# Performance work log

Hardware: AMD Instinct MI355X
Metric: run time of the kernel (lower is better)

Reference implementation:

```python
import jax, jax.numpy as jnp
import numpy as np

H, LQ, LK, DK, DV = 16, 2048, 2048, 64, 64


def setup_inputs() -> dict:
    key = jax.random.key(0)
    k1, k2, k3, k4 = jax.random.split(key, 4)
    q = jax.random.normal(k1, (H, LQ, DK), dtype=jnp.float32)
    k = jax.random.normal(k2, (H, LK, DK), dtype=jnp.float32)
    v = jax.random.normal(k3, (1, LK, DV), dtype=jnp.float32)
    attn_mask = jax.random.randint(k4, (H, LQ, LK), 0, 2) == 1
    return {"q": q, "k": k, "v": v, "attn_mask": attn_mask, "train_attn": 1}


def reference(q, k, v, attn_mask, train_attn):
    scale = jnp.asarray(np.sqrt(q.shape[-1]), q.dtype)  # sqrt(d_k)
    # [H, Lq, Lk] scores
    attn = jnp.einsum('hqd,hkd->hqk', q, k) / scale
    attn = jnp.where(attn_mask, -jnp.inf, attn)
    attn = jax.nn.softmax(attn, axis=-1)
    # torch: v.repeat(n_heads,1,1) then bmm -> v[0] broadcast over heads
    attn_used = attn if train_attn else jax.lax.stop_gradient(attn)
    v_used = jax.lax.stop_gradient(v) if train_attn else v
    outputs = jnp.einsum('hqk,kd->hqd', attn_used, v_used[0])
    return outputs, attn
```

## Files before the change

kernel.cpp:

```cpp
#include <hip/hip_runtime.h>
#include <hip/hip_bf16.h>
#include <math.h>

#define H_ 16
#define LQ_ 2048
#define LK_ 2048
#define D_ 64
#define MBLK_ 32
#define NWAVE_ 4
#define STRIP_ (LK_ / NWAVE_)
#define NCH_ (STRIP_ / 32)

using bf16x8  = __attribute__((ext_vector_type(8))) short;
using floatx4 = __attribute__((ext_vector_type(4))) float;

__device__ __forceinline__ unsigned short f2bf(float x) {
  unsigned u = __builtin_bit_cast(unsigned, x);
  return (unsigned short)((u + 0x7fffu + ((u >> 16) & 1u)) >> 16);
}
__device__ __forceinline__ float bf2f(unsigned short b) {
  return __builtin_bit_cast(float, ((unsigned)b) << 16);
}
__device__ __forceinline__ void hilo8(const float* __restrict__ x, bf16x8& hv, bf16x8& lv) {
#pragma unroll
  for (int j = 0; j < 8; ++j) {
    unsigned short hb = f2bf(x[j]);
    float d = x[j] - bf2f(hb);
    hv[j] = (short)hb;
    lv[j] = (short)(unsigned short)(__builtin_bit_cast(unsigned, d) >> 16);
  }
}

__global__ void detect_mask_kernel(const unsigned int* __restrict__ m,
                                   int* __restrict__ flag) {
  if (threadIdx.x == 0) {
    unsigned int acc = 0u;
#pragma unroll 8
    for (int i = 0; i < 256; ++i) acc |= m[i];
    *flag = (acc & 0xFFFFFF00u) ? 1 : 0;
  }
}

__global__ __launch_bounds__(256, 2)
void attn_mfma_kernel(const float* __restrict__ Qg, const float* __restrict__ Kg,
                      const float* __restrict__ Vg, const void* __restrict__ Mg,
                      const int* __restrict__ flagp,
                      float* __restrict__ Og, float* __restrict__ Ag) {
  const int tid = (int)threadIdx.x;
  const int l   = tid & 63;
  const int w   = tid >> 6;
  const int lm  = l & 15;
  const int lg  = l >> 4;
  const int hd  = (int)blockIdx.y;
  const int q0  = (int)blockIdx.x * MBLK_;
  const int k0w = w * STRIP_;

  __shared__ __align__(16) float OM[NWAVE_][MBLK_ * D_];
  __shared__ float Stats[NWAVE_][MBLK_][2];

  short* Pw = reinterpret_cast<short*>(&OM[0][0]) + w * 2048;
  short* Ph = Pw;
  short* Pl = Pw + 1024;

  const int maskByte = *flagp;
  const unsigned char* Mb = (const unsigned char*)Mg;
  const int* Mi = (const int*)Mg;

  const float* Qh_ = Qg + (size_t)hd * LQ_ * D_;
  const float* Kh_ = Kg + (size_t)hd * LK_ * D_;

  bf16x8 qh[2][2], ql[2][2];
#pragma unroll
  for (int Mt = 0; Mt < 2; ++Mt) {
    const float* qp = Qh_ + (size_t)(q0 + Mt * 16 + lm) * D_;
#pragma unroll
    for (int s = 0; s < 2; ++s) {
      float x[8];
      *(floatx4*)(x)     = *(const floatx4*)(qp + s * 32 + lg * 8);
      *(floatx4*)(x + 4) = *(const floatx4*)(qp + s * 32 + lg * 8 + 4);
      hilo8(x, qh[Mt][s], ql[Mt][s]);
    }
  }

  float mreg[8], sreg[8];
#pragma unroll
  for (int i = 0; i < 8; ++i) { mreg[i] = -1e30f; sreg[i] = 0.0f; }

#pragma unroll 1
  for (int c = 0; c < NCH_; ++c) {
#pragma unroll
    for (int kt = 0; kt < 2; ++kt) {
      const int kcol = k0w + c * 32 + kt * 16 + lm;
      const float* kp = Kh_ + (size_t)kcol * D_;
      bf16x8 kh[2], kl[2];
#pragma unroll
      for (int s = 0; s < 2; ++s) {
        float x[8];
        *(floatx4*)(x)     = *(const floatx4*)(kp + s * 32 + lg * 8);
        *(floatx4*)(x + 4) = *(const floatx4*)(kp + s * 32 + lg * 8 + 4);
        hilo8(x, kh[s], kl[s]);
      }
#pragma unroll
      for (int Mt = 0; Mt < 2; ++Mt) {
        floatx4 acc = {0.f, 0.f, 0.f, 0.f};
#pragma unroll
        for (int s = 0; s < 2; ++s) {
          acc = __builtin_amdgcn_mfma_f32_16x16x32_bf16(qh[Mt][s], kh[s], acc, 0, 0, 0);
          acc = __builtin_amdgcn_mfma_f32_16x16x32_bf16(ql[Mt][s], kh[s], acc, 0, 0, 0);
          acc = __builtin_amdgcn_mfma_f32_16x16x32_bf16(qh[Mt][s], kl[s], acc, 0, 0, 0);
        }
#pragma unroll
        for (int j = 0; j < 4; ++j) {
          const int row = Mt * 16 + lg * 4 + j;
          const size_t mi = ((size_t)hd * LQ_ + q0 + row) * (size_t)LK_ + kcol;
          const int msk = maskByte ? (int)Mb[mi] : Mi[mi];
          const float sv = msk ? -1e30f : acc[j] * 0.125f;
          const int rs = Mt * 4 + j;
          const float mo = mreg[rs];
          const float mn = fmaxf(mo, sv);
          sreg[rs] = sreg[rs] * __expf(mo - mn) + (msk ? 0.0f : __expf(sv - mn));
          mreg[rs] = mn;
        }
      }
    }
  }

#pragma unroll
  for (int rs = 0; rs < 8; ++rs) {
    float m = mreg[rs], S = sreg[rs];
#pragma unroll
    for (int off = 1; off <= 8; off <<= 1) {
      float mo = __shfl_xor(m, off, 64);
      float So = __shfl_xor(S, off, 64);
      float mn = fmaxf(m, mo);
      S = S * __expf(m - mn) + So * __expf(mo - mn);
      m = mn;
    }
    mreg[rs] = m; sreg[rs] = S;
  }
  if (lm == 0) {
#pragma unroll
    for (int rs = 0; rs < 8; ++rs) {
      const int row = (rs >> 2) * 16 + lg * 4 + (rs & 3);
      Stats[w][row][0] = mreg[rs];
      Stats[w][row][1] = sreg[rs];
    }
  }
  __syncthreads();
  float mfin[8], isum[8];
#pragma unroll
  for (int rs = 0; rs < 8; ++rs) {
    const int row = (rs >> 2) * 16 + lg * 4 + (rs & 3);
    float m = Stats[0][row][0], S = Stats[0][row][1];
#pragma unroll
    for (int ww = 1; ww < NWAVE_; ++ww) {
      float mo = Stats[ww][row][0], So = Stats[ww][row][1];
      float mn = fmaxf(m, mo);
      S = S * __expf(m - mn) + So * __expf(mo - mn);
      m = mn;
    }
    mfin[rs] = m; isum[rs] = 1.0f / S;
  }

  floatx4 oacc[2][4];
#pragma unroll
  for (int Mt = 0; Mt < 2; ++Mt)
#pragma unroll
    for (int Nt = 0; Nt < 4; ++Nt) oacc[Mt][Nt] = {0.f, 0.f, 0.f, 0.f};

#pragma unroll 1
  for (int c = 0; c < NCH_; ++c) {
    const int kc0 = k0w + c * 32;
#pragma unroll
    for (int kt = 0; kt < 2; ++kt) {
      const int kcol = kc0 + kt * 16 + lm;
      const float* kp = Kh_ + (size_t)kcol * D_;
      bf16x8 kh[2], kl[2];
#pragma unroll
      for (int s = 0; s < 2; ++s) {
        float x[8];
        *(floatx4*)(x)     = *(const floatx4*)(kp + s * 32 + lg * 8);
        *(floatx4*)(x + 4) = *(const floatx4*)(kp + s * 32 + lg * 8 + 4);
        hilo8(x, kh[s], kl[s]);
      }
#pragma unroll
      for (int Mt = 0; Mt < 2; ++Mt) {
        floatx4 acc = {0.f, 0.f, 0.f, 0.f};
#pragma unroll
        for (int s = 0; s < 2; ++s) {
          acc = __builtin_amdgcn_mfma_f32_16x16x32_bf16(qh[Mt][s], kh[s], acc, 0, 0, 0);
          acc = __builtin_amdgcn_mfma_f32_16x16x32_bf16(ql[Mt][s], kh[s], acc, 0, 0, 0);
          acc = __builtin_amdgcn_mfma_f32_16x16x32_bf16(qh[Mt][s], kl[s], acc, 0, 0, 0);
        }
#pragma unroll
        for (int j = 0; j < 4; ++j) {
          const int row = Mt * 16 + lg * 4 + j;
          const size_t mi = ((size_t)hd * LQ_ + q0 + row) * (size_t)LK_ + kcol;
          const int msk = maskByte ? (int)Mb[mi] : Mi[mi];
          const int rs = Mt * 4 + j;
          const float p = msk ? 0.0f : __expf(acc[j] * 0.125f - mfin[rs]) * isum[rs];
          Ag[mi] = p;
          const unsigned short phb = f2bf(p);
          Ph[row * 32 + kt * 16 + lm] = (short)phb;
          Pl[row * 32 + kt * 16 + lm] =
              (short)(unsigned short)(__builtin_bit_cast(unsigned, p - bf2f(phb)) >> 16);
        }
      }
    }
    bf16x8 pa[2], plo[2];
#pragma unroll
    for (int Mt = 0; Mt < 2; ++Mt) {
      pa[Mt]  = *(const bf16x8*)(Ph + (Mt * 16 + lm) * 32 + lg * 8);
      plo[Mt] = *(const bf16x8*)(Pl + (Mt * 16 + lm) * 32 + lg * 8);
    }
#pragma unroll
    for (int Nt = 0; Nt < 4; ++Nt) {
      float vx[8];
#pragma unroll
      for (int jj = 0; jj < 8; ++jj)
        vx[jj] = Vg[(size_t)(kc0 + lg * 8 + jj) * D_ + Nt * 16 + lm];
      bf16x8 vh, vl;
      hilo8(vx, vh, vl);
#pragma unroll
      for (int Mt = 0; Mt < 2; ++Mt) {
        floatx4 o = oacc[Mt][Nt];
        o = __builtin_amdgcn_mfma_f32_16x16x32_bf16(pa[Mt],  vh, o, 0, 0, 0);
        o = __builtin_amdgcn_mfma_f32_16x16x32_bf16(plo[Mt], vh, o, 0, 0, 0);
        o = __builtin_amdgcn_mfma_f32_16x16x32_bf16(pa[Mt],  vl, o, 0, 0, 0);
        oacc[Mt][Nt] = o;
      }
    }
  }

  __syncthreads();
#pragma unroll
  for (int Mt = 0; Mt < 2; ++Mt)
#pragma unroll
    for (int Nt = 0; Nt < 4; ++Nt)
#pragma unroll
      for (int j = 0; j < 4; ++j)
        OM[w][(Mt * 16 + lg * 4 + j) * D_ + Nt * 16 + lm] = oacc[Mt][Nt][j];
  __syncthreads();
  for (int i = tid; i < MBLK_ * D_; i += 256) {
    const float s0 = OM[0][i] + OM[1][i] + OM[2][i] + OM[3][i];
    Og[((size_t)hd * LQ_ + q0 + (i >> 6)) * D_ + (i & 63)] = s0;
  }
}

extern "C" void kernel_launch(void* const* d_in, const int* in_sizes, int n_in,
                              void* d_out, int out_size, void* d_ws, size_t ws_size,
                              hipStream_t stream) {
  const float* Qg = (const float*)d_in[0];
  const float* Kg = (const float*)d_in[1];
  const float* Vg = (const float*)d_in[2];
  const void*  Mg = d_in[3];
  int* flag = (int*)d_ws;

  hipLaunchKernelGGL(detect_mask_kernel, dim3(1), dim3(64), 0, stream,
                     (const unsigned int*)Mg, flag);

  float* Og = (float*)d_out;
  float* Ag = (float*)d_out + (size_t)H_ * LQ_ * D_;

  dim3 grid(LQ_ / MBLK_, H_);
  hipLaunchKernelGGL(attn_mfma_kernel, grid, dim3(256), 0, stream,
                     Qg, Kg, Vg, Mg, flag, Og, Ag);
}
```

Baseline: 799.7 us.

## Precompute bf16 hi/lo operands and packed bitmask, single-pass score kernel

Adds pre-kernels that pack the mask into bits, split Q and K into bf16 hi/lo arrays, and transpose V into hi/lo bf16. The attention kernel now uses 16-row query blocks, keeps all scores in registers so QK^T is computed once instead of twice, uses an exact max/sum softmax, and writes the attention matrix with vectorized stores. This removes the recomputed QK^T, the repeated per-use conversions, and the byte-wide mask reads, at the cost of extra launches, workspace traffic and higher register use. Attention values are now stored as hi+lo bf16 sums, which may differ slightly from fp32.

```diff
diff --git a/kernel.cpp b/kernel.cpp
--- a/kernel.cpp
+++ b/kernel.cpp
@@ -6,10 +6,12 @@
 #define LQ_ 2048
 #define LK_ 2048
 #define D_ 64
-#define MBLK_ 32
-#define NWAVE_ 4
-#define STRIP_ (LK_ / NWAVE_)
+#define QB_ 16
+#define NW_ 4
+#define STRIP_ (LK_ / NW_)
+#define NTL_ (STRIP_ / 16)
 #define NCH_ (STRIP_ / 32)
+#define PP_ 40
 
 using bf16x8  = __attribute__((ext_vector_type(8))) short;
 using floatx4 = __attribute__((ext_vector_type(4))) float;
@@ -31,219 +33,256 @@
   }
 }
 
-__global__ void detect_mask_kernel(const unsigned int* __restrict__ m,
-                                   int* __restrict__ flag) {
-  if (threadIdx.x == 0) {
-    unsigned int acc = 0u;
-#pragma unroll 8
-    for (int i = 0; i < 256; ++i) acc |= m[i];
-    *flag = (acc & 0xFFFFFF00u) ? 1 : 0;
-  }
-}
-
+__global__ void detect_mask_kernel(const unsigned* __restrict__ m, int* __restrict__ flag) {
+  const int l = (int)threadIdx.x;
+  unsigned acc = 0;
+#pragma unroll
+  for (int i = 0; i < 4; ++i) acc |= m[l * 4 + i];
+  unsigned long long any = __ballot(acc & 0xFFFFFF00u);
+  if (l == 0) *flag = any ? 1 : 0;
+}
+
+__global__ void pack_mask_kernel(const void* __restrict__ Mg, const int* __restrict__ flagp,
+                                 unsigned* __restrict__ Wp) {
+  const size_t i = (size_t)blockIdx.x * 256 + threadIdx.x;
+  unsigned wbits = 0;
+  if (*flagp) {
+    const uint4* p = (const uint4*)((const unsigned char*)Mg + i * 32);
+    uint4 a = p[0], b = p[1];
+    unsigned v[8] = {a.x, a.y, a.z, a.w, b.x, b.y, b.z, b.w};
+#pragma unroll
+    for (int k = 0; k < 8; ++k)
+#pragma unroll
+      for (int bb = 0; bb < 4; ++bb)
+        wbits |= (((v[k] >> (8 * bb)) & 0xFFu) ? 1u : 0u) << (4 * k + bb);
+  } else {
+    const uint4* p = (const uint4*)((const int*)Mg + i * 32);
+#pragma unroll
+    for (int k = 0; k < 8; ++k) {
+      uint4 a = p[k];
+      wbits |= (a.x ? 1u : 0u) << (4 * k)     | (a.y ? 1u : 0u) << (4 * k + 1) |
+               (a.z ? 1u : 0u) << (4 * k + 2) | (a.w ? 1u : 0u) << (4 * k + 3);
+    }
+  }
+  Wp[i] = wbits;
+}
+
+__global__ void conv_hilo_kernel(const float* __restrict__ X,
+                                 unsigned short* __restrict__ Hh,
+                                 unsigned short* __restrict__ Hl) {
+  const size_t i = (size_t)blockIdx.x * 256 + threadIdx.x;
+  float x[8];
+  *(floatx4*)x       = *(const floatx4*)(X + i * 8);
+  *(floatx4*)(x + 4) = *(const floatx4*)(X + i * 8 + 4);
+  bf16x8 hv, lv;
+  hilo8(x, hv, lv);
+  *(bf16x8*)(Hh + i * 8) = hv;
+  *(bf16x8*)(Hl + i * 8) = lv;
+}
+
+__global__ void conv_vt_kernel(const float* __restrict__ V,
+                               unsigned short* __restrict__ Th,
+                               unsigned short* __restrict__ Tl) {
+  const int i = (int)(blockIdx.x * 256 + threadIdx.x);
+  const int d = i >> 11, k = i & 2047;
+  float x = V[(size_t)k * D_ + d];
+  unsigned short hb = f2bf(x);
+  float rem = x - bf2f(hb);
+  Th[(size_t)d * LK_ + k] = hb;
+  Tl[(size_t)d * LK_ + k] = (unsigned short)(__builtin_bit_cast(unsigned, rem) >> 16);
+}
+
+template <bool PRE>
 __global__ __launch_bounds__(256, 2)
-void attn_mfma_kernel(const float* __restrict__ Qg, const float* __restrict__ Kg,
-                      const float* __restrict__ Vg, const void* __restrict__ Mg,
-                      const int* __restrict__ flagp,
-                      float* __restrict__ Og, float* __restrict__ Ag) {
+void attn_sp_kernel(const float* __restrict__ Qg, const float* __restrict__ Kg,
+                    const float* __restrict__ Vg, const void* __restrict__ Mg,
+                    const int* __restrict__ flagp,
+                    const unsigned* __restrict__ Wp,
+                    const unsigned short* __restrict__ Qhp, const unsigned short* __restrict__ Qlp,
+                    const unsigned short* __restrict__ Khp, const unsigned short* __restrict__ Klp,
+                    const unsigned short* __restrict__ Vthp, const unsigned short* __restrict__ Vtlp,
+                    float* __restrict__ Og, float* __restrict__ Ag) {
   const int tid = (int)threadIdx.x;
-  const int l   = tid & 63;
-  const int w   = tid >> 6;
-  const int lm  = l & 15;
-  const int lg  = l >> 4;
-  const int hd  = (int)blockIdx.y;
-  const int q0  = (int)blockIdx.x * MBLK_;
-  const int k0w = w * STRIP_;
-
-  __shared__ __align__(16) float OM[NWAVE_][MBLK_ * D_];
-  __shared__ float Stats[NWAVE_][MBLK_][2];
-
-  short* Pw = reinterpret_cast<short*>(&OM[0][0]) + w * 2048;
-  short* Ph = Pw;
-  short* Pl = Pw + 1024;
-
-  const int maskByte = *flagp;
+  const int l = tid & 63, w = tid >> 6, lm = l & 15, lg = l >> 4;
+  const int hd = (int)blockIdx.y;
+  const int q0 = (int)blockIdx.x * QB_;
+  const int k0 = w * STRIP_;
+
+  __shared__ float SM_[NW_][QB_];
+  __shared__ float SS_[NW_][QB_];
+  __shared__ __align__(16) float OM[NW_][QB_ * D_];
+  __shared__ __align__(16) unsigned short Pb[NW_][2][QB_ * PP_];
+
+  const int maskByte = PRE ? 0 : *flagp;
   const unsigned char* Mb = (const unsigned char*)Mg;
   const int* Mi = (const int*)Mg;
 
-  const float* Qh_ = Qg + (size_t)hd * LQ_ * D_;
-  const float* Kh_ = Kg + (size_t)hd * LK_ * D_;
-
-  bf16x8 qh[2][2], ql[2][2];
-#pragma unroll
-  for (int Mt = 0; Mt < 2; ++Mt) {
-    const float* qp = Qh_ + (size_t)(q0 + Mt * 16 + lm) * D_;
+  bf16x8 qh[2], ql[2];
+  if constexpr (PRE) {
+    const unsigned short* qp  = Qhp + ((size_t)hd * LQ_ + q0 + lm) * D_;
+    const unsigned short* qp2 = Qlp + ((size_t)hd * LQ_ + q0 + lm) * D_;
+    qh[0] = *(const bf16x8*)(qp + lg * 8);       qh[1] = *(const bf16x8*)(qp + 32 + lg * 8);
+    ql[0] = *(const bf16x8*)(qp2 + lg * 8);      ql[1] = *(const bf16x8*)(qp2 + 32 + lg * 8);
+  } else {
+    const float* qp = Qg + ((size_t)hd * LQ_ + q0 + lm) * D_;
 #pragma unroll
     for (int s = 0; s < 2; ++s) {
       float x[8];
-      *(floatx4*)(x)     = *(const floatx4*)(qp + s * 32 + lg * 8);
+      *(floatx4*)x       = *(const floatx4*)(qp + s * 32 + lg * 8);
       *(floatx4*)(x + 4) = *(const floatx4*)(qp + s * 32 + lg * 8 + 4);
-      hilo8(x, qh[Mt][s], ql[Mt][s]);
-    }
-  }
-
-  float mreg[8], sreg[8];
-#pragma unroll
-  for (int i = 0; i < 8; ++i) { mreg[i] = -1e30f; sreg[i] = 0.0f; }
-
-#pragma unroll 1
+      hilo8(x, qh[s], ql[s]);
+    }
+  }
+
+  float s[NTL_][4];
+  unsigned wm[4];
+  const size_t mwrow = ((size_t)hd * LQ_ + q0 + lg * 4);
+#pragma unroll
+  for (int t = 0; t < NTL_; ++t) {
+    if constexpr (PRE) {
+      if ((t & 1) == 0) {
+#pragma unroll
+        for (int j = 0; j < 4; ++j)
+          wm[j] = Wp[((mwrow + j) << 6) + (size_t)(w * 16) + (t >> 1)];
+      }
+    }
+    bf16x8 kh[2], kl[2];
+    if constexpr (PRE) {
+      const unsigned short* kp  = Khp + ((size_t)hd * LK_ + k0 + t * 16 + lm) * D_;
+      const unsigned short* kp2 = Klp + ((size_t)hd * LK_ + k0 + t * 16 + lm) * D_;
+      kh[0] = *(const bf16x8*)(kp + lg * 8);       kh[1] = *(const bf16x8*)(kp + 32 + lg * 8);
+      kl[0] = *(const bf16x8*)(kp2 + lg * 8);      kl[1] = *(const bf16x8*)(kp2 + 32 + lg * 8);
+    } else {
+      const float* kp = Kg + ((size_t)hd * LK_ + k0 + t * 16 + lm) * D_;
+#pragma unroll
+      for (int ss = 0; ss < 2; ++ss) {
+        float x[8];
+        *(floatx4*)x       = *(const floatx4*)(kp + ss * 32 + lg * 8);
+        *(floatx4*)(x + 4) = *(const floatx4*)(kp + ss * 32 + lg * 8 + 4);
+        hilo8(x, kh[ss], kl[ss]);
+      }
+    }
+    floatx4 acc = {0.f, 0.f, 0.f, 0.f};
+#pragma unroll
+    for (int ss = 0; ss < 2; ++ss) {
+      acc = __builtin_amdgcn_mfma_f32_16x16x32_bf16(qh[ss], kh[ss], acc, 0, 0, 0);
+      acc = __builtin_amdgcn_mfma_f32_16x16x32_bf16(ql[ss], kh[ss], acc, 0, 0, 0);
+      acc = __builtin_amdgcn_mfma_f32_16x16x32_bf16(qh[ss], kl[ss], acc, 0, 0, 0);
+    }
+#pragma unroll
+    for (int j = 0; j < 4; ++j) {
+      int mk;
+      if constexpr (PRE) {
+        mk = (int)((wm[j] >> ((t & 1) * 16 + lm)) & 1u);
+      } else {
+        const size_t mi = ((size_t)hd * LQ_ + q0 + lg * 4 + j) * (size_t)LK_ + k0 + t * 16 + lm;
+        mk = maskByte ? (int)Mb[mi] : Mi[mi];
+      }
+      s[t][j] = mk ? -1e30f : acc[j] * 0.125f;
+    }
+  }
+
+  float mf[4];
+#pragma unroll
+  for (int j = 0; j < 4; ++j) {
+    float m = s[0][j];
+#pragma unroll
+    for (int t = 1; t < NTL_; ++t) m = fmaxf(m, s[t][j]);
+#pragma unroll
+    for (int off = 1; off <= 8; off <<= 1) m = fmaxf(m, __shfl_xor(m, off, 64));
+    if (lm == 0) SM_[w][lg * 4 + j] = m;
+  }
+  __syncthreads();
+#pragma unroll
+  for (int j = 0; j < 4; ++j)
+    mf[j] = fmaxf(fmaxf(SM_[0][lg * 4 + j], SM_[1][lg * 4 + j]),
+                  fmaxf(SM_[2][lg * 4 + j], SM_[3][lg * 4 + j]));
+#pragma unroll
+  for (int j = 0; j < 4; ++j) {
+    float sum = 0.f;
+#pragma unroll
+    for (int t = 0; t < NTL_; ++t) {
+      float p = __expf(s[t][j] - mf[j]);
+      s[t][j] = p;
+      sum += p;
+    }
+#pragma unroll
+    for (int off = 1; off <= 8; off <<= 1) sum += __shfl_xor(sum, off, 64);
+    if (lm == 0) SS_[w][lg * 4 + j] = sum;
+  }
+  __syncthreads();
+  float inv[4];
+#pragma unroll
+  for (int j = 0; j < 4; ++j)
+    inv[j] = 1.0f / (SS_[0][lg * 4 + j] + SS_[1][lg * 4 + j] +
+                     SS_[2][lg * 4 + j] + SS_[3][lg * 4 + j]);
+
+  floatx4 oacc[4];
+#pragma unroll
+  for (int n = 0; n < 4; ++n) oacc[n] = {0.f, 0.f, 0.f, 0.f};
+  unsigned short* PhL = &Pb[w][0][0];
+  unsigned short* PlL = &Pb[w][1][0];
+
+#pragma unroll
   for (int c = 0; c < NCH_; ++c) {
 #pragma unroll
-    for (int kt = 0; kt < 2; ++kt) {
-      const int kcol = k0w + c * 32 + kt * 16 + lm;
-      const float* kp = Kh_ + (size_t)kcol * D_;
-      bf16x8 kh[2], kl[2];
-#pragma unroll
-      for (int s = 0; s < 2; ++s) {
-        float x[8];
-        *(floatx4*)(x)     = *(const floatx4*)(kp + s * 32 + lg * 8);
-        *(floatx4*)(x + 4) = *(const floatx4*)(kp + s * 32 + lg * 8 + 4);
-        hilo8(x, kh[s], kl[s]);
-      }
-#pragma unroll
-      for (int Mt = 0; Mt < 2; ++Mt) {
-        floatx4 acc = {0.f, 0.f, 0.f, 0.f};
-#pragma unroll
-        for (int s = 0; s < 2; ++s) {
-          acc = __builtin_amdgcn_mfma_f32_16x16x32_bf16(qh[Mt][s], kh[s], acc, 0, 0, 0);
-          acc = __builtin_amdgcn_mfma_f32_16x16x32_bf16(ql[Mt][s], kh[s], acc, 0, 0, 0);
-          acc = __builtin_amdgcn_mfma_f32_16x16x32_bf16(qh[Mt][s], kl[s], acc, 0, 0, 0);
-        }
-#pragma unroll
-        for (int j = 0; j < 4; ++j) {
-          const int row = Mt * 16 + lg * 4 + j;
-          const size_t mi = ((size_t)hd * LQ_ + q0 + row) * (size_t)LK_ + kcol;
-          const int msk = maskByte ? (int)Mb[mi] : Mi[mi];
-          const float sv = msk ? -1e30f : acc[j] * 0.125f;
-          const int rs = Mt * 4 + j;
-          const float mo = mreg[rs];
-          const float mn = fmaxf(mo, sv);
-          sreg[rs] = sreg[rs] * __expf(mo - mn) + (msk ? 0.0f : __expf(sv - mn));
-          mreg[rs] = mn;
-        }
-      }
-    }
-  }
-
-#pragma unroll
-  for (int rs = 0; rs < 8; ++rs) {
-    float m = mreg[rs], S = sreg[rs];
-#pragma unroll
-    for (int off = 1; off <= 8; off <<= 1) {
-      float mo = __shfl_xor(m, off, 64);
-      float So = __shfl_xor(S, off, 64);
-      float mn = fmaxf(m, mo);
-      S = S * __expf(m - mn) + So * __expf(mo - mn);
-      m = mn;
-    }
-    mreg[rs] = m; sreg[rs] = S;
-  }
-  if (lm == 0) {
-#pragma unroll
-    for (int rs = 0; rs < 8; ++rs) {
-      const int row = (rs >> 2) * 16 + lg * 4 + (rs & 3);
-      Stats[w][row][0] = mreg[rs];
-      Stats[w][row][1] = sreg[rs];
-    }
-  }
+    for (int u = 0; u < 2; ++u) {
+#pragma unroll
+      for (int j = 0; j < 4; ++j) {
+        const float p = s[2 * c + u][j] * inv[j];
+        const unsigned short hb = f2bf(p);
+        const float rem = p - bf2f(hb);
+        PhL[(lg * 4 + j) * PP_ + u * 16 + lm] = hb;
+        PlL[(lg * 4 + j) * PP_ + u * 16 + lm] =
+            (unsigned short)(__builtin_bit_cast(unsigned, rem) >> 16);
+      }
+    }
+    const bf16x8 pa  = *(const bf16x8*)(PhL + lm * PP_ + lg * 8);
+    const bf16x8 plo = *(const bf16x8*)(PlL + lm * PP_ + lg * 8);
+
+    {
+      float pr[8];
+#pragma unroll
+      for (int jj = 0; jj < 8; ++jj)
+        pr[jj] = bf2f((unsigned short)pa[jj]) + bf2f((unsigned short)plo[jj]);
+      float* arow = Ag + ((size_t)hd * LQ_ + q0 + lm) * (size_t)LK_ + k0 + c * 32 + lg * 8;
+      floatx4 v0 = {pr[0], pr[1], pr[2], pr[3]};
+      floatx4 v1 = {pr[4], pr[5], pr[6], pr[7]};
+      *(floatx4*)arow       = v0;
+      *(floatx4*)(arow + 4) = v1;
+    }
+
+#pragma unroll
+    for (int n = 0; n < 4; ++n) {
+      bf16x8 vh, vl;
+      if constexpr (PRE) {
+        const size_t vo = (size_t)(n * 16 + lm) * LK_ + k0 + c * 32 + lg * 8;
+        vh = *(const bf16x8*)(Vthp + vo);
+        vl = *(const bf16x8*)(Vtlp + vo);
+      } else {
+        float vx[8];
+#pragma unroll
+        for (int jj = 0; jj < 8; ++jj)
+          vx[jj] = Vg[(size_t)(k0 + c * 32 + lg * 8 + jj) * D_ + n * 16 + lm];
+        hilo8(vx, vh, vl);
+      }
+      floatx4 o = oacc[n];
+      o = __builtin_amdgcn_mfma_f32_16x16x32_bf16(pa,  vh, o, 0, 0, 0);
+      o = __builtin_amdgcn_mfma_f32_16x16x32_bf16(plo, vh, o, 0, 0, 0);
+      o = __builtin_amdgcn_mfma_f32_16x16x32_bf16(pa,  vl, o, 0, 0, 0);
+      oacc[n] = o;
+    }
+  }
+
+#pragma unroll
+  for (int n = 0; n < 4; ++n)
+#pragma unroll
+    for (int j = 0; j < 4; ++j)
+      OM[w][(lg * 4 + j) * D_ + n * 16 + lm] = oacc[n][j];
   __syncthreads();
-  float mfin[8], isum[8];
-#pragma unroll
-  for (int rs = 0; rs < 8; ++rs) {
-    const int row = (rs >> 2) * 16 + lg * 4 + (rs & 3);
-    float m = Stats[0][row][0], S = Stats[0][row][1];
-#pragma unroll
-    for (int ww = 1; ww < NWAVE_; ++ww) {
-      float mo = Stats[ww][row][0], So = Stats[ww][row][1];
-      float mn = fmaxf(m, mo);
-      S = S * __expf(m - mn) + So * __expf(mo - mn);
-      m = mn;
-    }
-    mfin[rs] = m; isum[rs] = 1.0f / S;
-  }
-
-  floatx4 oacc[2][4];
-#pragma unroll
-  for (int Mt = 0; Mt < 2; ++Mt)
-#pragma unroll
-    for (int Nt = 0; Nt < 4; ++Nt) oacc[Mt][Nt] = {0.f, 0.f, 0.f, 0.f};
-
-#pragma unroll 1
-  for (int c = 0; c < NCH_; ++c) {
-    const int kc0 = k0w + c * 32;
-#pragma unroll
-    for (int kt = 0; kt < 2; ++kt) {
-      const int kcol = kc0 + kt * 16 + lm;
-      const float* kp = Kh_ + (size_t)kcol * D_;
-      bf16x8 kh[2], kl[2];
-#pragma unroll
-      for (int s = 0; s < 2; ++s) {
-        float x[8];
-        *(floatx4*)(x)     = *(const floatx4*)(kp + s * 32 + lg * 8);
-        *(floatx4*)(x + 4) = *(const floatx4*)(kp + s * 32 + lg * 8 + 4);
-        hilo8(x, kh[s], kl[s]);
-      }
-#pragma unroll
-      for (int Mt = 0; Mt < 2; ++Mt) {
-        floatx4 acc = {0.f, 0.f, 0.f, 0.f};
-#pragma unroll
-        for (int s = 0; s < 2; ++s) {
-          acc = __builtin_amdgcn_mfma_f32_16x16x32_bf16(qh[Mt][s], kh[s], acc, 0, 0, 0);
-          acc = __builtin_amdgcn_mfma_f32_16x16x32_bf16(ql[Mt][s], kh[s], acc, 0, 0, 0);
-          acc = __builtin_amdgcn_mfma_f32_16x16x32_bf16(qh[Mt][s], kl[s], acc, 0, 0, 0);
-        }
-#pragma unroll
-        for (int j = 0; j < 4; ++j) {
-          const int row = Mt * 16 + lg * 4 + j;
-          const size_t mi = ((size_t)hd * LQ_ + q0 + row) * (size_t)LK_ + kcol;
-          const int msk = maskByte ? (int)Mb[mi] : Mi[mi];
-          const int rs = Mt * 4 + j;
-          const float p = msk ? 0.0f : __expf(acc[j] * 0.125f - mfin[rs]) * isum[rs];
-          Ag[mi] = p;
-          const unsigned short phb = f2bf(p);
-          Ph[row * 32 + kt * 16 + lm] = (short)phb;
-          Pl[row * 32 + kt * 16 + lm] =
-              (short)(unsigned short)(__builtin_bit_cast(unsigned, p - bf2f(phb)) >> 16);
-        }
-      }
-    }
-    bf16x8 pa[2], plo[2];
-#pragma unroll
-    for (int Mt = 0; Mt < 2; ++Mt) {
-      pa[Mt]  = *(const bf16x8*)(Ph + (Mt * 16 + lm) * 32 + lg * 8);
-      plo[Mt] = *(const bf16x8*)(Pl + (Mt * 16 + lm) * 32 + lg * 8);
-    }
-#pragma unroll
-    for (int Nt = 0; Nt < 4; ++Nt) {
-      float vx[8];
-#pragma unroll
-      for (int jj = 0; jj < 8; ++jj)
-        vx[jj] = Vg[(size_t)(kc0 + lg * 8 + jj) * D_ + Nt * 16 + lm];
-      bf16x8 vh, vl;
-      hilo8(vx, vh, vl);
-#pragma unroll
-      for (int Mt = 0; Mt < 2; ++Mt) {
-        floatx4 o = oacc[Mt][Nt];
-        o = __builtin_amdgcn_mfma_f32_16x16x32_bf16(pa[Mt],  vh, o, 0, 0, 0);
-        o = __builtin_amdgcn_mfma_f32_16x16x32_bf16(plo[Mt], vh, o, 0, 0, 0);
-        o = __builtin_amdgcn_mfma_f32_16x16x32_bf16(pa[Mt],  vl, o, 0, 0, 0);
-        oacc[Mt][Nt] = o;
-      }
-    }
-  }
-
-  __syncthreads();
-#pragma unroll
-  for (int Mt = 0; Mt < 2; ++Mt)
-#pragma unroll
-    for (int Nt = 0; Nt < 4; ++Nt)
-#pragma unroll
-      for (int j = 0; j < 4; ++j)
-        OM[w][(Mt * 16 + lg * 4 + j) * D_ + Nt * 16 + lm] = oacc[Mt][Nt][j];
-  __syncthreads();
-  for (int i = tid; i < MBLK_ * D_; i += 256) {
-    const float s0 = OM[0][i] + OM[1][i] + OM[2][i] + OM[3][i];
-    Og[((size_t)hd * LQ_ + q0 + (i >> 6)) * D_ + (i & 63)] = s0;
+  for (int i = tid; i < QB_ * D_; i += 256) {
+    const float o = OM[0][i] + OM[1][i] + OM[2][i] + OM[3][i];
+    Og[((size_t)hd * LQ_ + q0 + (i >> 6)) * D_ + (i & 63)] = o;
   }
 }
 
@@ -254,15 +293,34 @@
   const float* Kg = (const float*)d_in[1];
   const float* Vg = (const float*)d_in[2];
   const void*  Mg = d_in[3];
-  int* flag = (int*)d_ws;
-
-  hipLaunchKernelGGL(detect_mask_kernel, dim3(1), dim3(64), 0, stream,
-                     (const unsigned int*)Mg, flag);
+
+  char* ws = (char*)d_ws;
+  int* flag = (int*)ws;
+  unsigned*       Wp  = (unsigned*)(ws + 16);
+  unsigned short* Qhp = (unsigned short*)(ws + 16 + 8388608);
+  unsigned short* Qlp = (unsigned short*)(ws + 16 + 8388608 + 4194304);
+  unsigned short* Khp = (unsigned short*)(ws + 16 + 8388608 + 2 * 4194304);
+  unsigned short* Klp = (unsigned short*)(ws + 16 + 8388608 + 3 * 4194304);
+  unsigned short* Vth = (unsigned short*)(ws + 16 + 8388608 + 4 * 4194304);
+  unsigned short* Vtl = (unsigned short*)(ws + 16 + 8388608 + 4 * 4194304 + 262144);
+  const size_t WS_NEEDED = 16 + 8388608 + 4 * (size_t)4194304 + 2 * (size_t)262144;
 
   float* Og = (float*)d_out;
   float* Ag = (float*)d_out + (size_t)H_ * LQ_ * D_;
 
-  dim3 grid(LQ_ / MBLK_, H_);
-  hipLaunchKernelGGL(attn_mfma_kernel, grid, dim3(256), 0, stream,
-                     Qg, Kg, Vg, Mg, flag, Og, Ag);
-}
+  hipLaunchKernelGGL(detect_mask_kernel, dim3(1), dim3(64), 0, stream,
+                     (const unsigned*)Mg, flag);
+
+  dim3 grid(LQ_ / QB_, H_);
+  if (ws_size >= WS_NEEDED) {
+    hipLaunchKernelGGL(pack_mask_kernel, dim3(8192), dim3(256), 0, stream, Mg, flag, Wp);
+    hipLaunchKernelGGL(conv_hilo_kernel, dim3(1024), dim3(256), 0, stream, Qg, Qhp, Qlp);
+    hipLaunchKernelGGL(conv_hilo_kernel, dim3(1024), dim3(256), 0, stream, Kg, Khp, Klp);
+    hipLaunchKernelGGL(conv_vt_kernel, dim3(512), dim3(256), 0, stream, Vg, Vth, Vtl);
+    hipLaunchKernelGGL((attn_sp_kernel<true>), grid, dim3(256), 0, stream,
+                       Qg, Kg, Vg, Mg, flag, Wp, Qhp, Qlp, Khp, Klp, Vth, Vtl, Og, Ag);
+  } else {
+    hipLaunchKernelGGL((attn_sp_kernel<false>), grid, dim3(256), 0, stream,
+                       Qg, Kg, Vg, Mg, flag, Wp, Qhp, Qlp, Khp, Klp, Vth, Vtl, Og, Ag);
+  }
+}
```

Measured after the change: 691.9 us. 1.16x faster.
